# Optimization experiments

Hardware: AMD Instinct MI355X
Metric: run time of the kernel (lower is better)

The kernel has to match this reference:

```python
import jax, jax.numpy as jnp
import numpy as np

B, S, D, H, DH = 8, 1024, 768, 12, 64
INIT_STD = 0.02
IGNORE = -100000.0


def setup_inputs() -> dict:
    key = jax.random.key(0)
    ks = jax.random.split(key, 5)
    return {
        "normalized_resid_pre": jax.random.normal(ks[0], (B, S, D), dtype=jnp.float32),
        "W_Q": jax.random.normal(ks[1], (H, D, DH), dtype=jnp.float32) * INIT_STD,
        "b_Q": jnp.zeros((H, DH), dtype=jnp.float32),
        "W_K": jax.random.normal(ks[2], (H, D, DH), dtype=jnp.float32) * INIT_STD,
        "b_K": jnp.zeros((H, DH), dtype=jnp.float32),
        "W_V": jax.random.normal(ks[3], (H, D, DH), dtype=jnp.float32) * INIT_STD,
        "b_V": jnp.zeros((H, DH), dtype=jnp.float32),
        "W_O": jax.random.normal(ks[4], (H, DH, D), dtype=jnp.float32) * INIT_STD,
        "b_O": jnp.zeros((D,), dtype=jnp.float32),
    }


def reference(normalized_resid_pre, W_Q, b_Q, W_K, b_K, W_V, b_V, W_O, b_O):
    x = normalized_resid_pre  # [B,S,D]
    q = jnp.einsum('bsd,hde->bshe', x, W_Q) + b_Q  # [B,S,H,DH]
    k = jnp.einsum('bsd,hde->bshe', x, W_K) + b_K
    v = jnp.einsum('bsd,hde->bshe', x, W_V) + b_V
    scores = jnp.einsum('bqhe,bkhe->bhqk', q, k) / jnp.sqrt(jnp.float32(DH))
    causal = jnp.triu(jnp.ones((S, S), dtype=bool), k=1)  # True above diagonal
    scores = jnp.where(causal, jnp.float32(IGNORE), scores)
    pattern = jax.nn.softmax(scores, axis=-1)  # [B,H,S,S]
    z = jnp.einsum('bhqk,bkhe->bqhe', pattern, v)  # [B,S,H,DH]
    attn_out = jnp.einsum('bqhe,hed->bqd', z, W_O) + b_O  # [B,S,D]
    return attn_out
```

## Files before the change

kernel.cpp:

```cpp
#include <hip/hip_runtime.h>
#include <hip/hip_bf16.h>
#include <stdint.h>

#define BB 8
#define SS 1024
#define DD 768
#define HH 12
#define DHH 64
#define BS (BB*SS)
#define NQKV (3*HH*DHH)

typedef __attribute__((ext_vector_type(8))) short bf16x8;
typedef __attribute__((ext_vector_type(4))) float f32x4;
typedef __attribute__((ext_vector_type(4))) unsigned int u32x4;

typedef const __attribute__((address_space(1))) unsigned int gu32;
typedef __attribute__((address_space(3))) unsigned int lu32;

static __device__ __forceinline__ unsigned short f2bf(float f) {
    union { float f; unsigned int u; } v; v.f = f;
    unsigned int u = v.u;
    unsigned int r = (u + 0x7fffu + ((u >> 16) & 1u)) >> 16;
    return (unsigned short)r;
}

static __device__ __forceinline__ unsigned int cvt_pk_bf16(float lo, float hi) {
    unsigned int r;
    asm("v_cvt_pk_bf16_f32 %0, %1, %2" : "=v"(r) : "v"(lo), "v"(hi));
    return r;
}


__global__ void k_f32_to_bf16(const float* __restrict__ in, unsigned short* __restrict__ out, int n) {
    int i = (blockIdx.x * 256 + threadIdx.x) * 4;
    if (i + 3 < n) {
        float4 v = *reinterpret_cast<const float4*>(in + i);
        ushort4 o;
        o.x = f2bf(v.x); o.y = f2bf(v.y); o.z = f2bf(v.z); o.w = f2bf(v.w);
        *reinterpret_cast<ushort4*>(out + i) = o;
    } else {
        for (; i < n; ++i) out[i] = f2bf(in[i]);
    }
}

__global__ void k_transpose_wqkv(const float* __restrict__ wq, const float* __restrict__ wk,
                                 const float* __restrict__ wv, unsigned short* __restrict__ wt) {
    __shared__ float tl[64][65];
    int rt = blockIdx.x;
    int z = blockIdx.y;
    int mat = z / 12, h = z - mat * 12;
    const float* src = ((mat == 0) ? wq : (mat == 1) ? wk : wv) + (size_t)h * 768 * 64;
    int d0 = rt * 64;
    int t = threadIdx.x;
    int row = t >> 4, c4 = (t & 15) * 4;
    #pragma unroll
    for (int p = 0; p < 4; ++p) {
        int d = p * 16 + row;
        float4 v = *reinterpret_cast<const float4*>(&src[(size_t)(d0 + d) * 64 + c4]);
        tl[d][c4 + 0] = v.x; tl[d][c4 + 1] = v.y; tl[d][c4 + 2] = v.z; tl[d][c4 + 3] = v.w;
    }
    __syncthreads();
    unsigned short* dstb = wt + ((size_t)(mat * 768 + h * 64)) * 768;
    #pragma unroll
    for (int p = 0; p < 4; ++p) {
        int e = p * 16 + row;
        ushort4 o;
        o.x = f2bf(tl[c4 + 0][e]); o.y = f2bf(tl[c4 + 1][e]);
        o.z = f2bf(tl[c4 + 2][e]); o.w = f2bf(tl[c4 + 3][e]);
        *reinterpret_cast<ushort4*>(&dstb[(size_t)e * 768 + d0 + c4]) = o;
    }
}

__global__ void k_transpose_wo(const float* __restrict__ wo, unsigned short* __restrict__ wot) {
    __shared__ float tl[64][65];
    int r0 = blockIdx.x * 64;
    int c0 = blockIdx.y * 64;
    int t = threadIdx.x;
    int row = t >> 4, c4 = (t & 15) * 4;
    #pragma unroll
    for (int p = 0; p < 4; ++p) {
        int r = p * 16 + row;
        float4 v = *reinterpret_cast<const float4*>(&wo[(size_t)(r0 + r) * 768 + c0 + c4]);
        tl[r][c4 + 0] = v.x; tl[r][c4 + 1] = v.y; tl[r][c4 + 2] = v.z; tl[r][c4 + 3] = v.w;
    }
    __syncthreads();
    #pragma unroll
    for (int p = 0; p < 4; ++p) {
        int c = p * 16 + row;
        ushort4 o;
        o.x = f2bf(tl[c4 + 0][c]); o.y = f2bf(tl[c4 + 1][c]);
        o.z = f2bf(tl[c4 + 2][c]); o.w = f2bf(tl[c4 + 3][c]);
        *reinterpret_cast<ushort4*>(&wot[(size_t)(c0 + c) * 768 + r0 + c4]) = o;
    }
}

__global__ void k_transpose_v(const unsigned short* __restrict__ vb, unsigned short* __restrict__ vtb) {
    __shared__ unsigned short tl[64][68];
    int s0 = blockIdx.x * 64;
    int bh = blockIdx.y;
    const unsigned short* src = vb + (size_t)bh * SS * DHH;
    unsigned short* dst = vtb + (size_t)bh * DHH * SS;
    int t = threadIdx.x;
    #pragma unroll
    for (int i = 0; i < 16; ++i) {
        int idx = t + i * 256;
        int sl = idx >> 6, e = idx & 63;
        tl[sl][e] = src[(size_t)(s0 + sl) * DHH + e];
    }
    __syncthreads();
    #pragma unroll
    for (int i = 0; i < 16; ++i) {
        int idx = t + i * 256;
        int e = idx >> 6, sl = idx & 63;
        dst[(size_t)e * SS + s0 + sl] = tl[sl][e];
    }
}


__launch_bounds__(256)
__global__ void k_gemm_qkv(const unsigned short* __restrict__ xb,
                           const unsigned short* __restrict__ wt,
                           const float* __restrict__ bq, const float* __restrict__ bk,
                           const float* __restrict__ bv,
                           unsigned short* __restrict__ qb,
                           unsigned short* __restrict__ kb,
                           unsigned short* __restrict__ vb) {
    __shared__ unsigned short As[2][128 * 32];
    __shared__ unsigned short Bs[2][128 * 32];
    int r0 = blockIdx.x * 128;
    int c0 = blockIdx.y * 128;
    int t = threadIdx.x;
    int w = t >> 6, l = t & 63;
    int lr = l & 15, lg = l >> 4;
    int wr = w >> 1, wc = w & 1;
    int srow = l >> 2;
    int g8 = (((l & 3) - (l >> 3)) & 3) * 8;
    int rdo = ((lg + (lr >> 1)) & 3) * 8;

    f32x4 acc[4][4] = {};
    for (int kk = 0; kk < 12; ++kk) {
        int k0 = kk * 64;
        __syncthreads();
        #pragma unroll
        for (int c = 0; c < 2; ++c) {
            int seg = w * 2 + c;
            int row = seg * 16 + srow;
            #pragma unroll
            for (int hf = 0; hf < 2; ++hf) {
                __builtin_amdgcn_global_load_lds(
                    (gu32*)(xb + (size_t)(r0 + row) * DD + k0 + hf * 32 + g8),
                    (lu32*)&As[hf][seg * 512], 16, 0, 0);
                __builtin_amdgcn_global_load_lds(
                    (gu32*)(wt + (size_t)(c0 + row) * DD + k0 + hf * 32 + g8),
                    (lu32*)&Bs[hf][seg * 512], 16, 0, 0);
            }
        }
        __syncthreads();
        #pragma unroll
        for (int hf = 0; hf < 2; ++hf) {
            bf16x8 af[4], bfr[4];
            #pragma unroll
            for (int m = 0; m < 4; ++m)
                af[m] = *reinterpret_cast<const bf16x8*>(&As[hf][(wr * 64 + m * 16 + lr) * 32 + rdo]);
            #pragma unroll
            for (int n = 0; n < 4; ++n)
                bfr[n] = *reinterpret_cast<const bf16x8*>(&Bs[hf][(wc * 64 + n * 16 + lr) * 32 + rdo]);
            #pragma unroll
            for (int m = 0; m < 4; ++m)
                #pragma unroll
                for (int n = 0; n < 4; ++n)
                    acc[m][n] = __builtin_amdgcn_mfma_f32_16x16x32_bf16(af[m], bfr[n], acc[m][n], 0, 0, 0);
        }
    }
    #pragma unroll
    for (int n = 0; n < 4; ++n) {
        int c = c0 + wc * 64 + n * 16 + lr;
        int mat = c / 768;
        int within = c - mat * 768;
        int h = within >> 6, e = within & 63;
        const float* bptr = (mat == 0) ? bq : (mat == 1) ? bk : bv;
        float bias = bptr[within];
        unsigned short* dst = (mat == 0) ? qb : (mat == 1) ? kb : vb;
        #pragma unroll
        for (int m = 0; m < 4; ++m) {
            #pragma unroll
            for (int i = 0; i < 4; ++i) {
                int r = r0 + wr * 64 + m * 16 + lg * 4 + i;
                int b_ = r >> 10, s_ = r & 1023;
                dst[(((size_t)(b_ * HH + h)) * SS + s_) * DHH + e] = f2bf(acc[m][n][i] + bias);
            }
        }
    }
}


#define PW 34

__launch_bounds__(256, 3)
__global__ void k_attn(const unsigned short* __restrict__ qb,
                       const unsigned short* __restrict__ kb,
                       const unsigned short* __restrict__ vtb,
                       unsigned short* __restrict__ zb) {
    __shared__ unsigned short Ks[2][64 * 64];
    __shared__ unsigned short Vs[2][64 * 64];
    __shared__ unsigned int Pl[4][16 * PW];
    int id = blockIdx.x;
    int p = id / 96;
    int bh = id - p * 96;
    int qi = 15 - p;
    int q0 = qi * 64;

    int t = threadIdx.x, w = t >> 6, l = t & 63;
    int lr = l & 15, lg = l >> 4;
    const unsigned short* Qh = qb + (size_t)bh * SS * DHH;
    const unsigned short* Kh = kb + (size_t)bh * SS * DHH;
    const unsigned short* Vt = vtb + (size_t)bh * DHH * SS;
    int b_ = bh / HH, h = bh - b_ * HH;
    unsigned int* Pw = &Pl[w][0];

    int sr8 = l >> 3;
    int sc = ((l & 7) ^ sr8) * 8;

    auto STAGE = [&](int buf, int kbase) {
        #pragma unroll
        for (int c = 0; c < 2; ++c) {
            int seg = w * 2 + c;
            int row = seg * 8 + sr8;
            __builtin_amdgcn_global_load_lds(
                (gu32*)(Kh + (size_t)(kbase + row) * DHH + sc),
                (lu32*)&Ks[buf][seg * 512], 16, 0, 0);
            __builtin_amdgcn_global_load_lds(
                (gu32*)(Vt + (size_t)row * SS + kbase + sc),
                (lu32*)&Vs[buf][seg * 512], 16, 0, 0);
        }
    };

    int qabs = q0 + w * 16 + lr;
    STAGE(0, 0);
    bf16x8 qf[2];
    qf[0] = *reinterpret_cast<const bf16x8*>(Qh + (size_t)qabs * DHH + lg * 8);
    qf[1] = *reinterpret_cast<const bf16x8*>(Qh + (size_t)qabs * DHH + 32 + lg * 8);

    float m_r = -3.0e38f, l_r = 0.f;
    f32x4 zacc[4] = {};
    __syncthreads();

    for (int kt = 0; kt <= qi; ++kt) {
        int k0 = kt * 64;
        int cur = kt & 1;
        if (kt < qi) STAGE(cur ^ 1, k0 + 64);

        f32x4 sac[4] = {};
        #pragma unroll
        for (int ks = 0; ks < 2; ++ks) {
            #pragma unroll
            for (int ct = 0; ct < 4; ++ct) {
                bf16x8 kfr = *reinterpret_cast<const bf16x8*>(
                    &Ks[cur][(ct * 16 + lr) * 64 + (((ks * 4 + lg) ^ (lr & 7)) * 8)]);
                sac[ct] = __builtin_amdgcn_mfma_f32_16x16x32_bf16(kfr, qf[ks], sac[ct], 0, 0, 0);
            }
        }
        bool diag = (kt == qi);
        float sv[4][4];
        float pm = -3.0e38f;
        #pragma unroll
        for (int ct = 0; ct < 4; ++ct) {
            #pragma unroll
            for (int i = 0; i < 4; ++i) {
                float x = sac[ct][i] * 0.125f;
                if (diag) {
                    int kabs = k0 + ct * 16 + lg * 4 + i;
                    if (kabs > qabs) x = -3.0e38f;
                }
                sv[ct][i] = x;
                pm = fmaxf(pm, x);
            }
        }
        pm = fmaxf(pm, __shfl_xor(pm, 16));
        pm = fmaxf(pm, __shfl_xor(pm, 32));

        if (!__all(pm <= m_r + 8.f)) {
            float mn = fmaxf(m_r, pm);
            float alpha = __expf(m_r - mn);
            m_r = mn;
            l_r *= alpha;
            float aC[4];
            #pragma unroll
            for (int i = 0; i < 4; ++i) aC[i] = __shfl(alpha, lg * 4 + i);
            #pragma unroll
            for (int et = 0; et < 4; ++et)
                #pragma unroll
                for (int i = 0; i < 4; ++i) zacc[et][i] *= aC[i];
        }

        float ps = 0.f;
        #pragma unroll
        for (int ct = 0; ct < 4; ++ct) {
            float p0 = __expf(sv[ct][0] - m_r);
            float p1 = __expf(sv[ct][1] - m_r);
            float p2 = __expf(sv[ct][2] - m_r);
            float p3 = __expf(sv[ct][3] - m_r);
            ps += (p0 + p1) + (p2 + p3);
            unsigned int pk0 = cvt_pk_bf16(p0, p1);
            unsigned int pk1 = cvt_pk_bf16(p2, p3);
            *reinterpret_cast<uint2*>(&Pw[lr * PW + ct * 8 + lg * 2]) = make_uint2(pk0, pk1);
        }
        ps += __shfl_xor(ps, 16);
        ps += __shfl_xor(ps, 32);
        l_r += ps;

        #pragma unroll
        for (int ks = 0; ks < 2; ++ks) {
            bf16x8 pa = *reinterpret_cast<const bf16x8*>(&Pw[lr * PW + ks * 16 + lg * 4]);
            #pragma unroll
            for (int et = 0; et < 4; ++et) {
                bf16x8 vf = *reinterpret_cast<const bf16x8*>(
                    &Vs[cur][(et * 16 + lr) * 64 + (((ks * 4 + lg) ^ (lr & 7)) * 8)]);
                zacc[et] = __builtin_amdgcn_mfma_f32_16x16x32_bf16(pa, vf, zacc[et], 0, 0, 0);
            }
        }
        __syncthreads();
    }

    float lC[4];
    #pragma unroll
    for (int i = 0; i < 4; ++i) lC[i] = __shfl(l_r, lg * 4 + i);
    #pragma unroll
    for (int et = 0; et < 4; ++et) {
        #pragma unroll
        for (int i = 0; i < 4; ++i) {
            int r = q0 + w * 16 + lg * 4 + i;
            float z = zacc[et][i] / lC[i];
            zb[((size_t)(b_ * SS + r)) * DD + h * DHH + et * 16 + lr] = f2bf(z);
        }
    }
}


__launch_bounds__(256)
__global__ void k_gemm_out(const unsigned short* __restrict__ zb,
                           const unsigned short* __restrict__ wot,
                           const float* __restrict__ bo,
                           float* __restrict__ out) {
    __shared__ unsigned short As[2][128 * 32];
    __shared__ unsigned short Bs[2][128 * 32];
    int r0 = blockIdx.x * 128;
    int c0 = blockIdx.y * 128;
    int t = threadIdx.x;
    int w = t >> 6, l = t & 63;
    int lr = l & 15, lg = l >> 4;
    int wr = w >> 1, wc = w & 1;
    int srow = l >> 2;
    int g8 = (((l & 3) - (l >> 3)) & 3) * 8;
    int rdo = ((lg + (lr >> 1)) & 3) * 8;

    f32x4 acc[4][4] = {};
    for (int kk = 0; kk < 12; ++kk) {
        int k0 = kk * 64;
        __syncthreads();
        #pragma unroll
        for (int c = 0; c < 2; ++c) {
            int seg = w * 2 + c;
            int row = seg * 16 + srow;
            #pragma unroll
            for (int hf = 0; hf < 2; ++hf) {
                __builtin_amdgcn_global_load_lds(
                    (gu32*)(zb + (size_t)(r0 + row) * DD + k0 + hf * 32 + g8),
                    (lu32*)&As[hf][seg * 512], 16, 0, 0);
                __builtin_amdgcn_global_load_lds(
                    (gu32*)(wot + (size_t)(c0 + row) * DD + k0 + hf * 32 + g8),
                    (lu32*)&Bs[hf][seg * 512], 16, 0, 0);
            }
        }
        __syncthreads();
        #pragma unroll
        for (int hf = 0; hf < 2; ++hf) {
            bf16x8 af[4], bfr[4];
            #pragma unroll
            for (int m = 0; m < 4; ++m)
                af[m] = *reinterpret_cast<const bf16x8*>(&As[hf][(wr * 64 + m * 16 + lr) * 32 + rdo]);
            #pragma unroll
            for (int n = 0; n < 4; ++n)
                bfr[n] = *reinterpret_cast<const bf16x8*>(&Bs[hf][(wc * 64 + n * 16 + lr) * 32 + rdo]);
            #pragma unroll
            for (int m = 0; m < 4; ++m)
                #pragma unroll
                for (int n = 0; n < 4; ++n)
                    acc[m][n] = __builtin_amdgcn_mfma_f32_16x16x32_bf16(af[m], bfr[n], acc[m][n], 0, 0, 0);
        }
    }
    #pragma unroll
    for (int n = 0; n < 4; ++n) {
        int c = c0 + wc * 64 + n * 16 + lr;
        float bias = bo[c];
        #pragma unroll
        for (int m = 0; m < 4; ++m) {
            #pragma unroll
            for (int i = 0; i < 4; ++i) {
                int r = r0 + wr * 64 + m * 16 + lg * 4 + i;
                out[(size_t)r * DD + c] = acc[m][n][i] + bias;
            }
        }
    }
}


extern "C" void kernel_launch(void* const* d_in, const int* in_sizes, int n_in,
                              void* d_out, int out_size, void* d_ws, size_t ws_size,
                              hipStream_t stream) {
    const float* x  = (const float*)d_in[0];
    const float* wq = (const float*)d_in[1];
    const float* bq = (const float*)d_in[2];
    const float* wk = (const float*)d_in[3];
    const float* bk = (const float*)d_in[4];
    const float* wv = (const float*)d_in[5];
    const float* bv = (const float*)d_in[6];
    const float* wo = (const float*)d_in[7];
    const float* bo = (const float*)d_in[8];
    float* out = (float*)d_out;

    char* ws = (char*)d_ws;
    size_t off = 0;
    auto alloc = [&](size_t bytes) -> char* {
        char* p = ws + off;
        off += (bytes + 255) & ~(size_t)255;
        return p;
    };
    unsigned short* xb   = (unsigned short*)alloc((size_t)BS * DD * 2);
    unsigned short* wt   = (unsigned short*)alloc((size_t)NQKV * DD * 2);
    unsigned short* wot  = (unsigned short*)alloc((size_t)DD * DD * 2);
    unsigned short* qb   = (unsigned short*)alloc((size_t)BB * HH * SS * DHH * 2);
    unsigned short* kb   = (unsigned short*)alloc((size_t)BB * HH * SS * DHH * 2);
    unsigned short* vb   = (unsigned short*)alloc((size_t)BB * HH * SS * DHH * 2);
    unsigned short* vtb  = (unsigned short*)alloc((size_t)BB * HH * SS * DHH * 2);
    unsigned short* zb   = (unsigned short*)alloc((size_t)BS * DD * 2);
    (void)ws_size; (void)in_sizes; (void)n_in; (void)out_size;

    k_f32_to_bf16<<<dim3((BS * DD) / (256 * 4)), dim3(256), 0, stream>>>(x, xb, BS * DD);
    k_transpose_wqkv<<<dim3(12, 36), dim3(256), 0, stream>>>(wq, wk, wv, wt);
    k_transpose_wo<<<dim3(12, 12), dim3(256), 0, stream>>>(wo, wot);
    k_gemm_qkv<<<dim3(BS / 128, NQKV / 128), dim3(256), 0, stream>>>(xb, wt, bq, bk, bv, qb, kb, vb);
    k_transpose_v<<<dim3(SS / 64, BB * HH), dim3(256), 0, stream>>>(vb, vtb);
    k_attn<<<dim3(16 * 96), dim3(256), 0, stream>>>(qb, kb, vtb, zb);
    k_gemm_out<<<dim3(BS / 128, DD / 128), dim3(256), 0, stream>>>(zb, wot, bo, out);
}
```

Before: 127.4 us.

## Double-buffer LDS tiles in QKV and output GEMMs with async prefetch

```diff
diff --git a/kernel.cpp b/kernel.cpp
--- a/kernel.cpp
+++ b/kernel.cpp
@@ -29,6 +29,10 @@
     asm("v_cvt_pk_bf16_f32 %0, %1, %2" : "=v"(r) : "v"(lo), "v"(hi));
     return r;
 }
+
+#define WAITBAR8() asm volatile("s_waitcnt vmcnt(8)\ns_barrier" ::: "memory")
+#define WAITBAR0() asm volatile("s_waitcnt vmcnt(0)\ns_barrier" ::: "memory")
+#define BAR()      asm volatile("s_barrier" ::: "memory")
 
 
 __global__ void k_f32_to_bf16(const float* __restrict__ in, unsigned short* __restrict__ out, int n) {
@@ -125,8 +129,8 @@
                            unsigned short* __restrict__ qb,
                            unsigned short* __restrict__ kb,
                            unsigned short* __restrict__ vb) {
-    __shared__ unsigned short As[2][128 * 32];
-    __shared__ unsigned short Bs[2][128 * 32];
+    __shared__ unsigned short As[2][2][128 * 32];
+    __shared__ unsigned short Bs[2][2][128 * 32];
     int r0 = blockIdx.x * 128;
     int c0 = blockIdx.y * 128;
     int t = threadIdx.x;
@@ -138,9 +142,8 @@
     int rdo = ((lg + (lr >> 1)) & 3) * 8;
 
     f32x4 acc[4][4] = {};
-    for (int kk = 0; kk < 12; ++kk) {
-        int k0 = kk * 64;
-        __syncthreads();
+
+    auto STAGE = [&](int buf, int k0) {
         #pragma unroll
         for (int c = 0; c < 2; ++c) {
             int seg = w * 2 + c;
@@ -149,29 +152,48 @@
             for (int hf = 0; hf < 2; ++hf) {
                 __builtin_amdgcn_global_load_lds(
                     (gu32*)(xb + (size_t)(r0 + row) * DD + k0 + hf * 32 + g8),
-                    (lu32*)&As[hf][seg * 512], 16, 0, 0);
+                    (lu32*)&As[buf][hf][seg * 512], 16, 0, 0);
                 __builtin_amdgcn_global_load_lds(
                     (gu32*)(wt + (size_t)(c0 + row) * DD + k0 + hf * 32 + g8),
-                    (lu32*)&Bs[hf][seg * 512], 16, 0, 0);
-            }
-        }
-        __syncthreads();
+                    (lu32*)&Bs[buf][hf][seg * 512], 16, 0, 0);
+            }
+        }
+    };
+    auto COMPUTE = [&](int buf) {
         #pragma unroll
         for (int hf = 0; hf < 2; ++hf) {
             bf16x8 af[4], bfr[4];
             #pragma unroll
             for (int m = 0; m < 4; ++m)
-                af[m] = *reinterpret_cast<const bf16x8*>(&As[hf][(wr * 64 + m * 16 + lr) * 32 + rdo]);
+                af[m] = *reinterpret_cast<const bf16x8*>(&As[buf][hf][(wr * 64 + m * 16 + lr) * 32 + rdo]);
             #pragma unroll
             for (int n = 0; n < 4; ++n)
-                bfr[n] = *reinterpret_cast<const bf16x8*>(&Bs[hf][(wc * 64 + n * 16 + lr) * 32 + rdo]);
+                bfr[n] = *reinterpret_cast<const bf16x8*>(&Bs[buf][hf][(wc * 64 + n * 16 + lr) * 32 + rdo]);
             #pragma unroll
             for (int m = 0; m < 4; ++m)
                 #pragma unroll
                 for (int n = 0; n < 4; ++n)
                     acc[m][n] = __builtin_amdgcn_mfma_f32_16x16x32_bf16(af[m], bfr[n], acc[m][n], 0, 0, 0);
         }
-    }
+    };
+
+    STAGE(0, 0);
+    for (int kk2 = 0; kk2 < 6; ++kk2) {
+        int k0 = kk2 * 128;
+        STAGE(1, k0 + 64);
+        WAITBAR8();
+        COMPUTE(0);
+        BAR();
+        if (kk2 < 5) {
+            STAGE(0, k0 + 128);
+            WAITBAR8();
+        } else {
+            WAITBAR0();
+        }
+        COMPUTE(1);
+        BAR();
+    }
+
     #pragma unroll
     for (int n = 0; n < 4; ++n) {
         int c = c0 + wc * 64 + n * 16 + lr;
@@ -342,8 +364,8 @@
                            const unsigned short* __restrict__ wot,
                            const float* __restrict__ bo,
                            float* __restrict__ out) {
-    __shared__ unsigned short As[2][128 * 32];
-    __shared__ unsigned short Bs[2][128 * 32];
+    __shared__ unsigned short As[2][2][128 * 32];
+    __shared__ unsigned short Bs[2][2][128 * 32];
     int r0 = blockIdx.x * 128;
     int c0 = blockIdx.y * 128;
     int t = threadIdx.x;
@@ -355,9 +377,8 @@
     int rdo = ((lg + (lr >> 1)) & 3) * 8;
 
     f32x4 acc[4][4] = {};
-    for (int kk = 0; kk < 12; ++kk) {
-        int k0 = kk * 64;
-        __syncthreads();
+
+    auto STAGE = [&](int buf, int k0) {
         #pragma unroll
         for (int c = 0; c < 2; ++c) {
             int seg = w * 2 + c;
@@ -366,29 +387,48 @@
             for (int hf = 0; hf < 2; ++hf) {
                 __builtin_amdgcn_global_load_lds(
                     (gu32*)(zb + (size_t)(r0 + row) * DD + k0 + hf * 32 + g8),
-                    (lu32*)&As[hf][seg * 512], 16, 0, 0);
+                    (lu32*)&As[buf][hf][seg * 512], 16, 0, 0);
                 __builtin_amdgcn_global_load_lds(
                     (gu32*)(wot + (size_t)(c0 + row) * DD + k0 + hf * 32 + g8),
-                    (lu32*)&Bs[hf][seg * 512], 16, 0, 0);
-            }
-        }
-        __syncthreads();
+                    (lu32*)&Bs[buf][hf][seg * 512], 16, 0, 0);
+            }
+        }
+    };
+    auto COMPUTE = [&](int buf) {
         #pragma unroll
         for (int hf = 0; hf < 2; ++hf) {
             bf16x8 af[4], bfr[4];
             #pragma unroll
             for (int m = 0; m < 4; ++m)
-                af[m] = *reinterpret_cast<const bf16x8*>(&As[hf][(wr * 64 + m * 16 + lr) * 32 + rdo]);
+                af[m] = *reinterpret_cast<const bf16x8*>(&As[buf][hf][(wr * 64 + m * 16 + lr) * 32 + rdo]);
             #pragma unroll
             for (int n = 0; n < 4; ++n)
-                bfr[n] = *reinterpret_cast<const bf16x8*>(&Bs[hf][(wc * 64 + n * 16 + lr) * 32 + rdo]);
+                bfr[n] = *reinterpret_cast<const bf16x8*>(&Bs[buf][hf][(wc * 64 + n * 16 + lr) * 32 + rdo]);
             #pragma unroll
             for (int m = 0; m < 4; ++m)
                 #pragma unroll
                 for (int n = 0; n < 4; ++n)
                     acc[m][n] = __builtin_amdgcn_mfma_f32_16x16x32_bf16(af[m], bfr[n], acc[m][n], 0, 0, 0);
         }
-    }
+    };
+
+    STAGE(0, 0);
+    for (int kk2 = 0; kk2 < 6; ++kk2) {
+        int k0 = kk2 * 128;
+        STAGE(1, k0 + 64);
+        WAITBAR8();
+        COMPUTE(0);
+        BAR();
+        if (kk2 < 5) {
+            STAGE(0, k0 + 128);
+            WAITBAR8();
+        } else {
+            WAITBAR0();
+        }
+        COMPUTE(1);
+        BAR();
+    }
+
     #pragma unroll
     for (int n = 0; n < 4; ++n) {
         int c = c0 + wc * 64 + n * 16 + lr;
```

Result: no change. 126.6 us (-0.6%).
